# Kernel optimization log

Hardware: AMD Instinct MI355X
Metric: run time of the kernel (lower is better)

## Reference

```python
import jax, jax.numpy as jnp
import numpy as np

B, D, H = 512, 256, 512

def setup_inputs() -> dict:
    key = jax.random.key(0)
    ks = jax.random.split(key, 7)
    s = lambda fan_in: 1.0 / np.sqrt(fan_in)
    return {
        "h": jax.random.normal(ks[0], (B, D), jnp.float32),
        "W1": jax.random.normal(ks[1], (2 * D, H), jnp.float32) * s(2 * D),
        "b1": jax.random.normal(ks[2], (H,), jnp.float32) * s(2 * D),
        "W2": jax.random.normal(ks[3], (H, H), jnp.float32) * s(H),
        "b2": jax.random.normal(ks[4], (H,), jnp.float32) * s(H),
        "W3": jax.random.normal(ks[5], (H, 1), jnp.float32) * s(H),
        "b3": jax.random.normal(ks[6], (1,), jnp.float32) * s(H),
    }

def reference(h, W1, b1, W2, b2, W3, b3):
    n = h.shape[0]
    # Split W1 into halves acting on hi and hj; equivalent to cat([hi,hj]) @ W1
    yi = h @ W1[:D]            # [B, H]
    yj = h @ W1[D:]            # [B, H]
    x = jnp.tanh(yi[:, None, :] + yj[None, :, :] + b1)   # [B, B, H]
    x = jnp.tanh(x @ W2 + b2)                             # [B, B, H]
    logits = (x @ W3 + b3)[..., 0]                        # [B, B]
    eye = jnp.eye(n, dtype=logits.dtype)
    return logits * (1.0 - eye) + (-20.0) * eye
```

## Files before the change

### kernel.cpp

```cpp
#include <hip/hip_runtime.h>
#include <cstdint>


#define NB 512
#define ND 256
#define NH 512
#define C2 2.885390081777927f

typedef int i32x4 __attribute__((ext_vector_type(4)));
typedef int i32x16 __attribute__((ext_vector_type(16)));
typedef unsigned int u32;
typedef unsigned char u8;

__device__ __forceinline__ float exp2_fast(float x) {
#if __has_builtin(__builtin_amdgcn_exp2f)
  return __builtin_amdgcn_exp2f(x);
#else
  return exp2f(x);
#endif
}
__device__ __forceinline__ float rcp_fast(float x) {
#if __has_builtin(__builtin_amdgcn_rcpf)
  return __builtin_amdgcn_rcpf(x);
#else
  return 1.0f / x;
#endif
}
__device__ __forceinline__ u32 perm_b32(u32 hi, u32 lo, u32 sel) {
#if __has_builtin(__builtin_amdgcn_perm)
  return __builtin_amdgcn_perm(hi, lo, sel);
#else
  u32 r = 0;
  for (int b = 0; b < 4; ++b) {
    const u32 c = (sel >> (8 * b)) & 255;
    const u32 byte = (c < 4) ? (lo >> (8 * c)) & 255 : (c < 8) ? (hi >> (8 * (c - 4))) & 255 : 0;
    r |= byte << (8 * b);
  }
  return r;
#endif
}
__device__ __forceinline__ u32 tanh_q127_magic(float u) {
  const float r = rcp_fast(exp2_fast(u) + 1.0f);
  return __builtin_bit_cast(u32, fmaf(-254.0f, r, 12583039.0f));
}

__device__ __forceinline__ float half32_sum(float s) {
#if __has_builtin(__builtin_amdgcn_update_dpp)
#define DPP_ADD(ctrl) \
  s += __builtin_bit_cast(float, __builtin_amdgcn_update_dpp(0, __builtin_bit_cast(int, s), ctrl, 0xF, 0xF, true))
  DPP_ADD(0x111);
  DPP_ADD(0x112);
  DPP_ADD(0x114);
  DPP_ADD(0x118);
  DPP_ADD(0x142);
#undef DPP_ADD
  return s;
#else
  for (int off = 1; off < 32; off <<= 1) s += __shfl_xor(s, off, 64);
  return s;
#endif
}

__global__ __launch_bounds__(256) void prep_all(const float* __restrict__ h,
                                                const float* __restrict__ W1,
                                                const float* __restrict__ b1,
                                                const float* __restrict__ W2,
                                                float* __restrict__ Ai,
                                                float* __restrict__ Aj,
                                                u8* __restrict__ W2q) {
  const int t = threadIdx.x;
  const int bx = blockIdx.x;
  if (bx < 512) {
    __shared__ float hs[16][68];
    __shared__ float w1t[64][36];
    __shared__ float w1b[64][36];
    const int it = bx >> 4, nt = bx & 15;
    const int i0 = it * 16, n0 = nt * 32;
    const int nn = t & 31, ig = t >> 5;
    float accA[2] = {0.f, 0.f}, accB[2] = {0.f, 0.f};
    for (int c2 = 0; c2 < 4; ++c2) {
      __syncthreads();
      {
        const int r = t >> 4, c0 = (t & 15) * 4;
        *(float4*)&hs[r][c0] = *(const float4*)(h + (size_t)(i0 + r) * ND + c2 * 64 + c0);
      }
      {
        const int r = t >> 2, c0 = (t & 3) * 8;
        const float* st = W1 + (size_t)(c2 * 64 + r) * NH + n0 + c0;
        const float* sb = W1 + (size_t)(256 + c2 * 64 + r) * NH + n0 + c0;
        const float4 a = *(const float4*)st;
        const float4 b = *(const float4*)(st + 4);
        const float4 c = *(const float4*)sb;
        const float4 d = *(const float4*)(sb + 4);
        *(float4*)&w1t[r][c0] = a;
        *(float4*)&w1t[r][c0 + 4] = b;
        *(float4*)&w1b[r][c0] = c;
        *(float4*)&w1b[r][c0 + 4] = d;
      }
      __syncthreads();
#pragma unroll 4
      for (int k4 = 0; k4 < 16; ++k4) {
        const float4 hv0 = *(const float4*)&hs[ig * 2 + 0][k4 * 4];
        const float4 hv1 = *(const float4*)&hs[ig * 2 + 1][k4 * 4];
        const float* h0 = (const float*)&hv0;
        const float* h1 = (const float*)&hv1;
#pragma unroll
        for (int j = 0; j < 4; ++j) {
          const float wtj = w1t[k4 * 4 + j][nn];
          const float wbj = w1b[k4 * 4 + j][nn];
          accA[0] = fmaf(h0[j], wtj, accA[0]);
          accA[1] = fmaf(h1[j], wtj, accA[1]);
          accB[0] = fmaf(h0[j], wbj, accB[0]);
          accB[1] = fmaf(h1[j], wbj, accB[1]);
        }
      }
    }
    const float b1n = b1[n0 + nn];
#pragma unroll
    for (int r = 0; r < 2; ++r) {
      Ai[(size_t)(i0 + ig * 2 + r) * NH + n0 + nn] = accA[r] * C2;
      Aj[(size_t)(i0 + ig * 2 + r) * NH + n0 + nn] = (accB[r] + b1n) * C2;
    }
  } else {
    const int g = (bx - 512) * 256 + t;
    const int lane = g & 63;
    const int nt = (g >> 6) & 15;
    const int ks = g >> 10;
    const int n = nt * 32 + (lane & 31);
    const int kb = ks * 32 + ((lane >> 5) << 4);
    u32 w[4];
#pragma unroll
    for (int q = 0; q < 4; ++q) {
      u32 acc = 0;
#pragma unroll
      for (int j = 0; j < 4; ++j) {
        const float wv = fminf(fmaxf(W2[(kb + q * 4 + j) * NH + n], -0.25f), 0.25f);
        const int qi = (int)rintf(wv * 508.0f);
        acc |= ((u32)(qi & 255)) << (8 * j);
      }
      w[q] = acc;
    }
    ((uint4*)W2q)[g] = make_uint4(w[0], w[1], w[2], w[3]);
  }
}

__global__ __launch_bounds__(512, 6) void pair_main(const float* __restrict__ Ai,
                                                    const float* __restrict__ Aj,
                                                    const u8* __restrict__ W2q,
                                                    const float* __restrict__ b2,
                                                    const float* __restrict__ W3,
                                                    const float* __restrict__ b3,
                                                    float* __restrict__ out) {
  __shared__ __align__(16) u8 xs[32 * 512];
  __shared__ float red[8][32];

  const int t = threadIdx.x;
  const int w = t >> 6;
  const int lane = t & 63;
  const int lhi = lane >> 5;
  const int llo = lane & 31;
  const int bx = blockIdx.x;
  const int i = bx >> 4;
  const int j0 = (bx & 15) * 32;

  i32x16 acc[2];
#pragma unroll
  for (int nt = 0; nt < 2; ++nt)
#pragma unroll
    for (int q = 0; q < 16; ++q) acc[nt][q] = 0;

  {
    const int row = t & 31;
    const int s0 = t >> 5;
    const float* ajr = Aj + (size_t)(j0 + row) * NH;
    const float* air = Ai + (size_t)i * NH;
#pragma unroll
    for (int uu = 0; uu < 2; ++uu) {
      const int s = s0 + uu * 16;
      const int k0 = s * 16;
      u32 wds[4];
#pragma unroll
      for (int q = 0; q < 4; ++q) {
        const float4 fa = *(const float4*)(ajr + k0 + q * 4);
        const float4 ga = *(const float4*)(air + k0 + q * 4);
        const u32 m0 = tanh_q127_magic(fa.x + ga.x);
        const u32 m1 = tanh_q127_magic(fa.y + ga.y);
        const u32 m2 = tanh_q127_magic(fa.z + ga.z);
        const u32 m3 = tanh_q127_magic(fa.w + ga.w);
        const u32 p01 = perm_b32(m1, m0, 0x0C0C0400u);
        const u32 p23 = perm_b32(m3, m2, 0x0C0C0400u);
        wds[q] = perm_b32(p23, p01, 0x05040100u);
      }
      ((uint4*)xs)[s * 32 + row] = make_uint4(wds[0], wds[1], wds[2], wds[3]);
    }
  }
  __syncthreads();

  const i32x4* xsv = (const i32x4*)xs;
  const int abase = lhi * 32 + llo;
  const uint4* w2v = (const uint4*)W2q + w * 128 + lane;

  i32x4 aP0 = xsv[abase];
  i32x4 aP1 = xsv[64 + abase];
  uint4 bP00 = w2v[0], bP01 = w2v[64];
  uint4 bP10 = w2v[1024], bP11 = w2v[1024 + 64];

#pragma unroll
  for (int kk = 0; kk < 8; ++kk) {
    const int ks0 = 2 * kk;
    {
      const i32x4 a = aP0;
      const i32x4 c0 = __builtin_bit_cast(i32x4, bP00);
      const i32x4 c1 = __builtin_bit_cast(i32x4, bP01);
      if (kk < 7) {
        aP0 = xsv[(ks0 + 2) * 64 + abase];
        const uint4* wp = w2v + (ks0 + 2) * 1024;
        bP00 = wp[0];
        bP01 = wp[64];
      }
      acc[0] = __builtin_amdgcn_mfma_i32_32x32x32_i8(a, c0, acc[0], 0, 0, 0);
      acc[1] = __builtin_amdgcn_mfma_i32_32x32x32_i8(a, c1, acc[1], 0, 0, 0);
    }
    {
      const i32x4 a = aP1;
      const i32x4 c0 = __builtin_bit_cast(i32x4, bP10);
      const i32x4 c1 = __builtin_bit_cast(i32x4, bP11);
      if (kk < 7) {
        aP1 = xsv[(ks0 + 3) * 64 + abase];
        const uint4* wp = w2v + (ks0 + 3) * 1024;
        bP10 = wp[0];
        bP11 = wp[64];
      }
      acc[0] = __builtin_amdgcn_mfma_i32_32x32x32_i8(a, c0, acc[0], 0, 0, 0);
      acc[1] = __builtin_amdgcn_mfma_i32_32x32x32_i8(a, c1, acc[1], 0, 0, 0);
    }
  }

  const float SCALE = (0.25f / (127.0f * 127.0f)) * C2;
  float b2c[2], w3v[2];
#pragma unroll
  for (int ntl = 0; ntl < 2; ++ntl) {
    const int n = w * 64 + ntl * 32 + llo;
    b2c[ntl] = b2[n] * C2;
    w3v[ntl] = W3[n];
  }
  const float w3s = half32_sum(w3v[0] + w3v[1]);

#pragma unroll
  for (int reg = 0; reg < 16; ++reg) {
    float sr = 0.0f;
#pragma unroll
    for (int ntl = 0; ntl < 2; ++ntl) {
      const float y = fmaf((float)acc[ntl][reg], SCALE, b2c[ntl]);
      const float r = rcp_fast(exp2_fast(y) + 1.0f);
      sr = fmaf(w3v[ntl], r, sr);
    }
    sr = half32_sum(sr);
    const int row = (reg & 3) + 8 * (reg >> 2) + 4 * lhi;
    if (llo == 31) red[w][row] = fmaf(-2.0f, sr, w3s);
  }
  __syncthreads();
  if (t < 32) {
    float v = b3[0];
#pragma unroll
    for (int ww = 0; ww < 8; ++ww) v += red[ww][t];
    const int j = j0 + t;
    out[i * NB + j] = (j == i) ? -20.0f : v;
  }
}

extern "C" void kernel_launch(void* const* d_in, const int* in_sizes, int n_in,
                              void* d_out, int out_size, void* d_ws, size_t ws_size,
                              hipStream_t stream) {
  const float* h = (const float*)d_in[0];
  const float* W1 = (const float*)d_in[1];
  const float* b1 = (const float*)d_in[2];
  const float* W2 = (const float*)d_in[3];
  const float* b2 = (const float*)d_in[4];
  const float* W3 = (const float*)d_in[5];
  const float* b3 = (const float*)d_in[6];
  float* out = (float*)d_out;

  float* Ai = (float*)d_ws;
  float* Aj = Ai + NB * NH;
  u8* W2q = (u8*)(Aj + NB * NH);

  prep_all<<<576, 256, 0, stream>>>(h, W1, b1, W2, Ai, Aj, W2q);
  pair_main<<<8192, 512, 0, stream>>>(Ai, Aj, W2q, b2, W3, b3, out);
}
```

Measured before the change: 216.5 us.

## Precompute exponentials per row and pair reciprocals to cut transcendental ops

The prep kernel now stores exp2 of the scaled row projections. The pair kernel therefore forms exp(a+b) as a product (fma with +1) and needs no exp per pair element. Reciprocals are computed two at a time, using rcp(e0*e1) times the other factor, which halves the rcp count in both the first tanh layer and the second-layer epilogue. The intent is to lower transcendental throughput pressure. The cost is extra multiplies and a possible overflow or inf risk when the product of exponentials is large.

```diff
diff --git a/kernel.cpp b/kernel.cpp
--- a/kernel.cpp
+++ b/kernel.cpp
@@ -39,8 +39,7 @@
   return r;
 #endif
 }
-__device__ __forceinline__ u32 tanh_q127_magic(float u) {
-  const float r = rcp_fast(exp2_fast(u) + 1.0f);
+__device__ __forceinline__ u32 tanh_magic_from_r(float r) {
   return __builtin_bit_cast(u32, fmaf(-254.0f, r, 12583039.0f));
 }
 
@@ -65,8 +64,8 @@
                                                 const float* __restrict__ W1,
                                                 const float* __restrict__ b1,
                                                 const float* __restrict__ W2,
-                                                float* __restrict__ Ai,
-                                                float* __restrict__ Aj,
+                                                float* __restrict__ Ei,
+                                                float* __restrict__ Ej,
                                                 u8* __restrict__ W2q) {
   const int t = threadIdx.x;
   const int bx = blockIdx.x;
@@ -118,8 +117,8 @@
     const float b1n = b1[n0 + nn];
 #pragma unroll
     for (int r = 0; r < 2; ++r) {
-      Ai[(size_t)(i0 + ig * 2 + r) * NH + n0 + nn] = accA[r] * C2;
-      Aj[(size_t)(i0 + ig * 2 + r) * NH + n0 + nn] = (accB[r] + b1n) * C2;
+      Ei[(size_t)(i0 + ig * 2 + r) * NH + n0 + nn] = exp2_fast(accA[r] * C2);
+      Ej[(size_t)(i0 + ig * 2 + r) * NH + n0 + nn] = exp2_fast((accB[r] + b1n) * C2);
     }
   } else {
     const int g = (bx - 512) * 256 + t;
@@ -144,8 +143,8 @@
   }
 }
 
-__global__ __launch_bounds__(512, 6) void pair_main(const float* __restrict__ Ai,
-                                                    const float* __restrict__ Aj,
+__global__ __launch_bounds__(512, 6) void pair_main(const float* __restrict__ Ei,
+                                                    const float* __restrict__ Ej,
                                                     const u8* __restrict__ W2q,
                                                     const float* __restrict__ b2,
                                                     const float* __restrict__ W3,
@@ -172,8 +171,8 @@
   {
     const int row = t & 31;
     const int s0 = t >> 5;
-    const float* ajr = Aj + (size_t)(j0 + row) * NH;
-    const float* air = Ai + (size_t)i * NH;
+    const float* ajr = Ej + (size_t)(j0 + row) * NH;
+    const float* air = Ei + (size_t)i * NH;
 #pragma unroll
     for (int uu = 0; uu < 2; ++uu) {
       const int s = s0 + uu * 16;
@@ -183,10 +182,16 @@
       for (int q = 0; q < 4; ++q) {
         const float4 fa = *(const float4*)(ajr + k0 + q * 4);
         const float4 ga = *(const float4*)(air + k0 + q * 4);
-        const u32 m0 = tanh_q127_magic(fa.x + ga.x);
-        const u32 m1 = tanh_q127_magic(fa.y + ga.y);
-        const u32 m2 = tanh_q127_magic(fa.z + ga.z);
-        const u32 m3 = tanh_q127_magic(fa.w + ga.w);
+        const float e0 = fmaf(fa.x, ga.x, 1.0f);
+        const float e1 = fmaf(fa.y, ga.y, 1.0f);
+        const float e2 = fmaf(fa.z, ga.z, 1.0f);
+        const float e3 = fmaf(fa.w, ga.w, 1.0f);
+        const float rp01 = rcp_fast(e0 * e1);
+        const float rp23 = rcp_fast(e2 * e3);
+        const u32 m0 = tanh_magic_from_r(e1 * rp01);
+        const u32 m1 = tanh_magic_from_r(e0 * rp01);
+        const u32 m2 = tanh_magic_from_r(e3 * rp23);
+        const u32 m3 = tanh_magic_from_r(e2 * rp23);
         const u32 p01 = perm_b32(m1, m0, 0x0C0C0400u);
         const u32 p23 = perm_b32(m3, m2, 0x0C0C0400u);
         wds[q] = perm_b32(p23, p01, 0x05040100u);
@@ -248,13 +253,14 @@
 
 #pragma unroll
   for (int reg = 0; reg < 16; ++reg) {
-    float sr = 0.0f;
-#pragma unroll
-    for (int ntl = 0; ntl < 2; ++ntl) {
-      const float y = fmaf((float)acc[ntl][reg], SCALE, b2c[ntl]);
-      const float r = rcp_fast(exp2_fast(y) + 1.0f);
-      sr = fmaf(w3v[ntl], r, sr);
-    }
+    const float y0 = fmaf((float)acc[0][reg], SCALE, b2c[0]);
+    const float y1 = fmaf((float)acc[1][reg], SCALE, b2c[1]);
+    const float e0 = exp2_fast(y0) + 1.0f;
+    const float e1 = exp2_fast(y1) + 1.0f;
+    const float rp = rcp_fast(e0 * e1);
+    const float r0 = e1 * rp;
+    const float r1 = e0 * rp;
+    float sr = fmaf(w3v[0], r0, w3v[1] * r1);
     sr = half32_sum(sr);
     const int row = (reg & 3) + 8 * (reg >> 2) + 4 * lhi;
     if (llo == 31) red[w][row] = fmaf(-2.0f, sr, w3s);
@@ -281,10 +287,10 @@
   const float* b3 = (const float*)d_in[6];
   float* out = (float*)d_out;
 
-  float* Ai = (float*)d_ws;
-  float* Aj = Ai + NB * NH;
-  u8* W2q = (u8*)(Aj + NB * NH);
-
-  prep_all<<<576, 256, 0, stream>>>(h, W1, b1, W2, Ai, Aj, W2q);
-  pair_main<<<8192, 512, 0, stream>>>(Ai, Aj, W2q, b2, W3, b3, out);
-}
+  float* Ei = (float*)d_ws;
+  float* Ej = Ei + NB * NH;
+  u8* W2q = (u8*)(Ej + NB * NH);
+
+  prep_all<<<576, 256, 0, stream>>>(h, W1, b1, W2, Ei, Ej, W2q);
+  pair_main<<<8192, 512, 0, stream>>>(Ei, Ej, W2q, b2, W3, b3, out);
+}
```

Measured after the change: 215.6 us. No clear change (-0.4%).
